# Optimization experiments

Measured on AMD Instinct MI355X. Metric: run time of the kernel, lower is better.

## Reference

```python
import jax, jax.numpy as jnp
import numpy as np
import math

B, S, H = 4, 1024, 1024
E, TOP_K, WINDOW = 4, 2, 64
CONFIGS = [(8, 'standard'), (12, 'standard'), (8, 'linear'), (8, 'local')]
PARAM_NAMES = ['Wq', 'bq', 'Wk', 'bk', 'Wv', 'bv', 'Wo', 'bo']


def setup_inputs() -> dict:
    key = jax.random.key(0)
    ks = jax.random.split(key, 2 + 8 * E)
    d = {}
    d['x'] = jax.random.normal(ks[0], (B, S, H), jnp.float32)
    d['Wg'] = jax.random.normal(ks[1], (H, E), jnp.float32) * 0.02
    i = 2
    for e, (nh, _) in enumerate(CONFIGS):
        hd = H // nh
        pd = nh * hd  # 1020 for nh=12, else 1024
        shapes = [(H, pd), (pd,), (H, pd), (pd,), (H, pd), (pd,), (pd, H), (H,)]
        for nm, shp in zip(PARAM_NAMES, shapes):
            d[f'e{e}_{nm}'] = jax.random.normal(ks[i], shp, jnp.float32) * 0.02
            i += 1
    d['attention_mask'] = jnp.ones((B, S), jnp.int32)
    return d


def _heads(y, nh, hd):
    b, s, _ = y.shape
    return y.reshape(b, s, nh, hd).transpose(0, 2, 1, 3)  # [b, nh, s, hd]


def _attention_expert(x, mask, Wq, bq, Wk, bk, Wv, bv, Wo, bo, nh, atype):
    b, s, _ = x.shape
    hd = Wq.shape[1] // nh
    scale = math.sqrt(hd)
    q = _heads(x @ Wq + bq, nh, hd)
    k = _heads(x @ Wk + bk, nh, hd)
    v = _heads(x @ Wv + bv, nh, hd)
    if atype == 'linear':
        # kernel-trick linear attention; original ignores attention_mask here
        q = jax.nn.elu(q) + 1.0
        k = jax.nn.elu(k) + 1.0
        kv = jnp.einsum('bhsd,bhse->bhde', k, v)
        num = jnp.einsum('bhqd,bhde->bhqe', q, kv)
        den = jnp.einsum('bhqd,bhd->bhq', q, k.sum(axis=2)) + 1e-6
        out = num / den[..., None]
    else:
        scores = jnp.einsum('bhqd,bhkd->bhqk', q, k) / scale
        if atype == 'local':
            idx = jnp.arange(s)
            dist = idx[None, :] - idx[:, None]  # j - i
            local_mask = jnp.abs(dist) <= WINDOW // 2
            scores = jnp.where(local_mask[None, None], scores, -jnp.inf)
        scores = jnp.where(mask[:, None, None, :] == 0, -jnp.inf, scores)
        probs = jax.nn.softmax(scores, axis=-1)
        probs = jnp.where(jnp.isnan(probs), 0.0, probs)  # nan_to_num(nan=0)
        out = jnp.einsum('bhqk,bhkd->bhqd', probs, v)
    out = out.transpose(0, 2, 1, 3).reshape(b, s, -1)
    return out @ Wo + bo


def _forward(x, Wg, eparams, attention_mask):
    b, s, h = x.shape
    # TopKGating (eval mode: no noise). logits -> top_k -> softmax over selected
    logits = x.reshape(-1, h) @ Wg  # [b*s, E]
    top_vals, top_idx = jax.lax.top_k(logits, TOP_K)
    gate_w = jax.nn.softmax(top_vals, axis=-1).reshape(b, s, TOP_K)
    sel = top_idx.reshape(b, s, TOP_K)
    outs = jnp.stack([
        _attention_expert(x, attention_mask, *eparams[e], CONFIGS[e][0], CONFIGS[e][1])
        for e in range(E)
    ], axis=0)  # [E, b, s, h]
    perm = outs.transpose(1, 2, 0, 3)  # [b, s, E, h]
    selected = jnp.take_along_axis(perm, sel[..., None], axis=2)  # [b, s, K, h]
    return (selected * gate_w[..., None]).sum(axis=2)


def reference(x, Wg,
              e0_Wq, e0_bq, e0_Wk, e0_bk, e0_Wv, e0_bv, e0_Wo, e0_bo,
              e1_Wq, e1_bq, e1_Wk, e1_bk, e1_Wv, e1_bv, e1_Wo, e1_bo,
              e2_Wq, e2_bq, e2_Wk, e2_bk, e2_Wv, e2_bv, e2_Wo, e2_bo,
              e3_Wq, e3_bq, e3_Wk, e3_bk, e3_Wv, e3_bv, e3_Wo, e3_bo,
              attention_mask):
    eparams = [
        (e0_Wq, e0_bq, e0_Wk, e0_bk, e0_Wv, e0_bv, e0_Wo, e0_bo),
        (e1_Wq, e1_bq, e1_Wk, e1_bk, e1_Wv, e1_bv, e1_Wo, e1_bo),
        (e2_Wq, e2_bq, e2_Wk, e2_bk, e2_Wv, e2_bv, e2_Wo, e2_bo),
        (e3_Wq, e3_bq, e3_Wk, e3_bk, e3_Wv, e3_bv, e3_Wo, e3_bo),
    ]
    return _forward(x, Wg, eparams, attention_mask)
```

## Files before the change

kernel.cpp:

```cpp
#include <hip/hip_runtime.h>
#include <cmath>

#define B_ 4
#define S_ 1024
#define H_ 1024

typedef short bf16x8 __attribute__((ext_vector_type(8)));
typedef float f32x4 __attribute__((ext_vector_type(4)));
typedef _Float16 half4 __attribute__((ext_vector_type(4)));

__device__ __forceinline__ unsigned short f2bf(float f) {
  unsigned u = __float_as_uint(f);
  u += 0x7fff + ((u >> 16) & 1);
  return (unsigned short)(u >> 16);
}
__device__ __forceinline__ float bf2f(unsigned short h) {
  return __uint_as_float(((unsigned)h) << 16);
}
__device__ __forceinline__ void gld16(const void* g, void* l) {
  __builtin_amdgcn_global_load_lds(
      (const __attribute__((address_space(1))) unsigned int*)g,
      (__attribute__((address_space(3))) unsigned int*)l, 16, 0, 0);
}

__global__ __launch_bounds__(64) void gate_kernel(
    const float* __restrict__ x, const float* __restrict__ Wg,
    float* __restrict__ gw) {
  int t = blockIdx.x;
  int lane = threadIdx.x;
  const float* xr = x + (size_t)t * H_;
  float a0 = 0.f, a1 = 0.f, a2 = 0.f, a3 = 0.f;
  for (int h = lane; h < H_; h += 64) {
    float xv = xr[h];
    const float* wr = Wg + h * 4;
    a0 += xv * wr[0]; a1 += xv * wr[1]; a2 += xv * wr[2]; a3 += xv * wr[3];
  }
  for (int off = 32; off > 0; off >>= 1) {
    a0 += __shfl_down(a0, off);
    a1 += __shfl_down(a1, off);
    a2 += __shfl_down(a2, off);
    a3 += __shfl_down(a3, off);
  }
  if (lane == 0) {
    float v[4] = {a0, a1, a2, a3};
    int i0 = 0; float b0 = v[0];
    for (int e = 1; e < 4; ++e) if (v[e] > b0) { b0 = v[e]; i0 = e; }
    int i1 = -1; float b1 = -INFINITY;
    for (int e = 0; e < 4; ++e) { if (e == i0) continue; if (v[e] > b1) { b1 = v[e]; i1 = e; } }
    float e1v = expf(b1 - b0);
    float w0 = 1.f / (1.f + e1v);
    float w1 = e1v / (1.f + e1v);
    float o[4] = {0.f, 0.f, 0.f, 0.f};
    o[i0] = w0; o[i1] = w1;
    float* g = gw + t * 4;
    g[0] = o[0]; g[1] = o[1]; g[2] = o[2]; g[3] = o[3];
  }
}

__global__ __launch_bounds__(256) void conv_kernel(
    const float* __restrict__ src, unsigned short* __restrict__ dst,
    int nsrc, int ldsrc) {
  int idx = blockIdx.x * 256 + threadIdx.x;
  int m = idx >> 10, c = idx & 1023;
  dst[idx] = (c < nsrc) ? f2bf(src[(size_t)m * ldsrc + c]) : (unsigned short)0;
}

__global__ __launch_bounds__(256) void wtrans4_kernel(
    const float* __restrict__ s0, const float* __restrict__ s1,
    const float* __restrict__ s2, const float* __restrict__ s3,
    unsigned short* __restrict__ d0, unsigned short* __restrict__ d1,
    unsigned short* __restrict__ d2, unsigned short* __restrict__ d3, int pd) {
  __shared__ float tile[32][33];
  int z = blockIdx.z;
  const float* src = (z == 0) ? s0 : (z == 1) ? s1 : (z == 2) ? s2 : s3;
  unsigned short* dst = (z == 0) ? d0 : (z == 1) ? d1 : (z == 2) ? d2 : d3;
  int ksrc = (z < 3) ? 1024 : pd;
  int nsrc = (z < 3) ? pd : 1024;
  int ldsrc = (z < 3) ? pd : 1024;
  int k0 = blockIdx.x * 32, n0 = blockIdx.y * 32;
  int tx = threadIdx.x & 31, ty = threadIdx.x >> 5;
  for (int i = 0; i < 32; i += 8) {
    int k = k0 + ty + i, n = n0 + tx;
    tile[ty + i][tx] = (k < ksrc && n < nsrc) ? src[(size_t)k * ldsrc + n] : 0.f;
  }
  __syncthreads();
  for (int i = 0; i < 32; i += 8) {
    int n = n0 + ty + i, k = k0 + tx;
    dst[(size_t)n * 1024 + k] = f2bf(tile[tx][ty + i]);
  }
}

__global__ __launch_bounds__(256) void gemm_mfma(
    const unsigned short* __restrict__ A, const unsigned short* __restrict__ Bt,
    const float* __restrict__ b0, const float* __restrict__ b1,
    const float* __restrict__ b2, void* __restrict__ Cv, int ldc,
    int nact, int elu_ncut, int out_bf16, int mode,
    const float* __restrict__ gw, int expert, int remap,
    int qs_ncut, float qscale) {
  constexpr int K = 1024;
  __shared__ __align__(16) unsigned short As[128 * 32];
  __shared__ __align__(16) unsigned short Bs[128 * 32];
  int tid = threadIdx.x, wave = tid >> 6, lane = tid & 63;
  int quad = lane >> 4, lrow = lane & 15;
  int rw = (wave >> 1) * 64, cw = (wave & 1) * 64;
  int m0 = blockIdx.y * 128, n0 = blockIdx.x * 128;
  int srow = wave * 32 + (lane >> 2);
  int scol = (lane & 3) * 8;
  const unsigned short* gA = A + (size_t)(m0 + srow) * K + scol;
  const unsigned short* gB = Bt + (size_t)(n0 + srow) * K + scol;
  unsigned short* lA = &As[wave * 1024];
  unsigned short* lB = &Bs[wave * 1024];
  f32x4 acc[4][4];
#pragma unroll
  for (int mt = 0; mt < 4; ++mt)
#pragma unroll
    for (int nt = 0; nt < 4; ++nt) acc[mt][nt] = (f32x4){0.f, 0.f, 0.f, 0.f};

  for (int k0 = 0; k0 < K; k0 += 32) {
    gld16(gA + k0, lA);
    gld16(gA + 16 * K + k0, lA + 512);
    gld16(gB + k0, lB);
    gld16(gB + 16 * K + k0, lB + 512);
    __syncthreads();
    bf16x8 af[4], bfr[4];
#pragma unroll
    for (int t = 0; t < 4; ++t) {
      af[t]  = *(const bf16x8*)&As[(rw + t * 16 + lrow) * 32 + quad * 8];
      bfr[t] = *(const bf16x8*)&Bs[(cw + t * 16 + lrow) * 32 + quad * 8];
    }
#pragma unroll
    for (int mt = 0; mt < 4; ++mt)
#pragma unroll
      for (int nt = 0; nt < 4; ++nt)
        acc[mt][nt] = __builtin_amdgcn_mfma_f32_16x16x32_bf16(
            af[mt], bfr[nt], acc[mt][nt], 0, 0, 0);
    __syncthreads();
  }
#pragma unroll
  for (int nt = 0; nt < 4; ++nt) {
    int n = n0 + cw + nt * 16 + lrow;
    int slice = n >> 10, noff = n & 1023;
    if (noff >= nact) continue;
    const float* bp = (slice == 0) ? b0 : (slice == 1) ? b1 : b2;
    float bias = bp[noff];
    bool do_elu = n < elu_ncut;
    bool do_qs = n < qs_ncut;
    int col = n;
    if (remap) {
      int head = (noff * 12337) >> 20;
      col = slice * 1152 + head * 96 + (noff - head * 85);
    }
#pragma unroll
    for (int mt = 0; mt < 4; ++mt) {
      int mb = m0 + rw + mt * 16 + quad * 4;
#pragma unroll
      for (int r = 0; r < 4; ++r) {
        int m = mb + r;
        float val = acc[mt][nt][r] + bias;
        if (do_elu) val = (val > 0.f) ? val + 1.f : expf(val);
        if (do_qs) val *= qscale;
        size_t ci = (size_t)m * ldc + col;
        if (out_bf16) {
          ((unsigned short*)Cv)[ci] = f2bf(val);
        } else {
          float* C = (float*)Cv;
          if (mode == 0) C[ci] = val;
          else {
            float g = gw[m * 4 + expert];
            if (mode == 1) C[ci] = g * val;
            else           C[ci] += g * val;
          }
        }
      }
    }
  }
}

struct OutP {
  const unsigned short* A[4];
  const unsigned short* B[4];
  const float* bias[4];
};

__global__ __launch_bounds__(256) void gemm_out4(
    OutP p, const float* __restrict__ gw, float* __restrict__ part) {
  constexpr int K = 1024;
  __shared__ __align__(16) unsigned short As[128 * 32];
  __shared__ __align__(16) unsigned short Bs[128 * 32];
  int e = blockIdx.z;
  const unsigned short* A = p.A[e];
  const unsigned short* Bt = p.B[e];
  const float* bp = p.bias[e];
  float* C = part + (size_t)e * (4096ull * 1024ull);
  int tid = threadIdx.x, wave = tid >> 6, lane = tid & 63;
  int quad = lane >> 4, lrow = lane & 15;
  int rw = (wave >> 1) * 64, cw = (wave & 1) * 64;
  int m0 = blockIdx.y * 128, n0 = blockIdx.x * 128;
  int srow = wave * 32 + (lane >> 2);
  int scol = (lane & 3) * 8;
  const unsigned short* gA = A + (size_t)(m0 + srow) * K + scol;
  const unsigned short* gB = Bt + (size_t)(n0 + srow) * K + scol;
  unsigned short* lA = &As[wave * 1024];
  unsigned short* lB = &Bs[wave * 1024];
  f32x4 acc[4][4];
#pragma unroll
  for (int mt = 0; mt < 4; ++mt)
#pragma unroll
    for (int nt = 0; nt < 4; ++nt) acc[mt][nt] = (f32x4){0.f, 0.f, 0.f, 0.f};

  for (int k0 = 0; k0 < K; k0 += 32) {
    gld16(gA + k0, lA);
    gld16(gA + 16 * K + k0, lA + 512);
    gld16(gB + k0, lB);
    gld16(gB + 16 * K + k0, lB + 512);
    __syncthreads();
    bf16x8 af[4], bfr[4];
#pragma unroll
    for (int t = 0; t < 4; ++t) {
      af[t]  = *(const bf16x8*)&As[(rw + t * 16 + lrow) * 32 + quad * 8];
      bfr[t] = *(const bf16x8*)&Bs[(cw + t * 16 + lrow) * 32 + quad * 8];
    }
#pragma unroll
    for (int mt = 0; mt < 4; ++mt)
#pragma unroll
      for (int nt = 0; nt < 4; ++nt)
        acc[mt][nt] = __builtin_amdgcn_mfma_f32_16x16x32_bf16(
            af[mt], bfr[nt], acc[mt][nt], 0, 0, 0);
    __syncthreads();
  }
#pragma unroll
  for (int nt = 0; nt < 4; ++nt) {
    int n = n0 + cw + nt * 16 + lrow;
    float bias = bp[n];
#pragma unroll
    for (int mt = 0; mt < 4; ++mt) {
      int mb = m0 + rw + mt * 16 + quad * 4;
#pragma unroll
      for (int r = 0; r < 4; ++r) {
        int m = mb + r;
        float g = gw[m * 4 + e];
        C[(size_t)m * 1024 + n] = g * (acc[mt][nt][r] + bias);
      }
    }
  }
}

__global__ __launch_bounds__(256) void reduce4(
    const float* __restrict__ part, float* __restrict__ out) {
  constexpr size_t N = 4096ull * 1024ull;
  size_t idx = ((size_t)blockIdx.x * 256 + threadIdx.x) * 4;
  f32x4 a0 = *(const f32x4*)(part + idx);
  f32x4 a1 = *(const f32x4*)(part + idx + N);
  f32x4 a2 = *(const f32x4*)(part + idx + 2 * N);
  f32x4 a3 = *(const f32x4*)(part + idx + 3 * N);
  f32x4 s;
#pragma unroll
  for (int j = 0; j < 4; ++j) {
    float t = a0[j];
    t += a1[j]; t += a2[j]; t += a3[j];
    s[j] = t;
  }
  *(f32x4*)(out + idx) = s;
}

__global__ __launch_bounds__(256) void padzero(
    unsigned short* __restrict__ qkv1, unsigned short* __restrict__ aob1) {
  int idx = blockIdx.x * 256 + threadIdx.x;
  int m = idx / 396, r = idx % 396;
  int slice = r / 132, r2 = r % 132;
  int head = r2 / 11, c = 85 + r2 % 11;
  qkv1[(size_t)m * 3456 + slice * 1152 + head * 96 + c] = 0;
  if (idx < 4096 * 4) {
    int mm = idx >> 2, cc = 1020 + (idx & 3);
    aob1[(size_t)mm * 1024 + cc] = 0;
  }
}

template <int HD, bool LOCAL>
__device__ __forceinline__ void attn_body(
    char* smem,
    const unsigned short* __restrict__ q, const unsigned short* __restrict__ k,
    const unsigned short* __restrict__ v, const int* __restrict__ amask,
    unsigned short* __restrict__ ao, int ldq, int h) {
  constexpr int HDP = (HD + 31) & ~31;
  constexpr int DCH = HDP / 32;
  constexpr int NDT = HDP / 16;
  constexpr int NCH = HDP / 8;
  constexpr int QT = 128, KT = 64;
  constexpr int KLD = HDP + 8;
  constexpr int VLD = KT + 4;
  constexpr int W2 = 32;
  unsigned short* Ks = (unsigned short*)smem;
  _Float16* Vt = (_Float16*)(smem + (size_t)KT * KLD * 2);
  unsigned long long* amq =
      (unsigned long long*)(smem + (size_t)KT * KLD * 2 + (size_t)HDP * VLD * 2);
  int tid = threadIdx.x, wave = tid >> 6, lane = tid & 63;
  int quad = lane >> 4, l15 = lane & 15;
  int q0 = blockIdx.x * QT, b = blockIdx.z;
  size_t baseq = ((size_t)b * S_) * ldq + (size_t)h * HDP;
  size_t baseo = ((size_t)b * S_) * H_ + (size_t)h * HD;

  {
    unsigned long long bb0 = __ballot(amask[b * S_ + wave * 128 + lane] != 0);
    unsigned long long bb1 = __ballot(amask[b * S_ + wave * 128 + 64 + lane] != 0);
    if (lane == 0) { amq[wave * 2] = bb0; amq[wave * 2 + 1] = bb1; }
  }

  int qrow = q0 + wave * 16 + l15;
  bf16x8 qf[DCH];
#pragma unroll
  for (int c = 0; c < DCH; ++c)
#pragma unroll
    for (int j = 0; j < 8; ++j) {
      int d = c * 32 + quad * 8 + j;
      qf[c][j] = (d < HD) ? (short)q[baseq + (size_t)qrow * ldq + d] : (short)0;
    }

  int jlo = 0, jhi = S_;
  if (LOCAL) {
    jlo = q0 - W2; if (jlo < 0) jlo = 0; jlo &= ~(KT - 1);
    jhi = q0 + QT + W2; if (jhi > S_) jhi = S_;
  }

  int skey = tid & 63, sc8a = tid >> 6, sc8b = 8 + (tid >> 6);
  bool sactb = sc8b < NCH;
  const unsigned short* kg = k + baseq + (size_t)skey * ldq;
  const unsigned short* vg = v + baseq + (size_t)skey * ldq;
  bf16x8 kra = {}, krb = {}, vra = {}, vrb = {};
  {
    size_t o = (size_t)jlo * ldq;
    kra = *(const bf16x8*)(kg + o + sc8a * 8);
    vra = *(const bf16x8*)(vg + o + sc8a * 8);
    if (sactb) {
      krb = *(const bf16x8*)(kg + o + sc8b * 8);
      vrb = *(const bf16x8*)(vg + o + sc8b * 8);
    }
  }

  float m_run = -1e30f, l_run = 0.f;
  f32x4 accd[NDT];
#pragma unroll
  for (int dt = 0; dt < NDT; ++dt) accd[dt] = (f32x4){0.f, 0.f, 0.f, 0.f};

  for (int j0 = jlo; j0 < jhi; j0 += KT) {
    __syncthreads();
    *(bf16x8*)&Ks[skey * KLD + sc8a * 8] = kra;
#pragma unroll
    for (int j = 0; j < 8; ++j)
      Vt[(sc8a * 8 + j) * VLD + skey] = (_Float16)bf2f((unsigned short)vra[j]);
    if (sactb) {
      *(bf16x8*)&Ks[skey * KLD + sc8b * 8] = krb;
#pragma unroll
      for (int j = 0; j < 8; ++j)
        Vt[(sc8b * 8 + j) * VLD + skey] = (_Float16)bf2f((unsigned short)vrb[j]);
    }
    __syncthreads();
    int jn = j0 + KT;
    if (jn < jhi) {
      size_t o = (size_t)jn * ldq;
      kra = *(const bf16x8*)(kg + o + sc8a * 8);
      vra = *(const bf16x8*)(vg + o + sc8a * 8);
      if (sactb) {
        krb = *(const bf16x8*)(kg + o + sc8b * 8);
        vrb = *(const bf16x8*)(vg + o + sc8b * 8);
      }
    }
    f32x4 sf[4];
#pragma unroll
    for (int kt = 0; kt < 4; ++kt) {
      sf[kt] = (f32x4){0.f, 0.f, 0.f, 0.f};
#pragma unroll
      for (int c = 0; c < DCH; ++c) {
        bf16x8 kf = *(const bf16x8*)&Ks[(kt * 16 + l15) * KLD + c * 32 + quad * 8];
        sf[kt] = __builtin_amdgcn_mfma_f32_16x16x32_bf16(kf, qf[c], sf[kt], 0, 0, 0);
      }
    }
    unsigned long long mb = amq[j0 >> 6];
    unsigned mw[2] = {(unsigned)mb, (unsigned)(mb >> 32)};
    float sval[4][4];
    bool vld[4][4];
    float mx = -1e30f;
#pragma unroll
    for (int kt = 0; kt < 4; ++kt) {
      unsigned word = mw[kt >> 1];
      int sh = (kt & 1) * 16 + quad * 4;
#pragma unroll
      for (int r = 0; r < 4; ++r) {
        bool ok = (word >> (sh + r)) & 1;
        if (LOCAL) {
          int dj = (j0 + kt * 16 + quad * 4 + r) - qrow;
          ok = ok && (dj <= W2) && (dj >= -W2);
        }
        float s = ok ? sf[kt][r] : -1e30f;
        sval[kt][r] = s;
        vld[kt][r] = ok;
        mx = fmaxf(mx, s);
      }
    }
    mx = fmaxf(mx, __shfl_xor(mx, 16));
    mx = fmaxf(mx, __shfl_xor(mx, 32));
    float m_new = fmaxf(m_run, mx);
    float psum = 0.f;
    float pv[4][4];
#pragma unroll
    for (int kt = 0; kt < 4; ++kt)
#pragma unroll
      for (int r = 0; r < 4; ++r) {
        float p = vld[kt][r] ? __builtin_amdgcn_exp2f(sval[kt][r] - m_new) : 0.f;
        pv[kt][r] = p;
        psum += p;
      }
    psum += __shfl_xor(psum, 16);
    psum += __shfl_xor(psum, 32);
    float alpha = __builtin_amdgcn_exp2f(m_run - m_new);
    m_run = m_new;
    l_run = l_run * alpha + psum;
    float aR[4];
#pragma unroll
    for (int r = 0; r < 4; ++r)
      aR[r] = __shfl(alpha, (lane & 48) | (quad * 4 + r));
#pragma unroll
    for (int dt = 0; dt < NDT; ++dt)
#pragma unroll
      for (int r = 0; r < 4; ++r) accd[dt][r] *= aR[r];
    half4 pf[4];
#pragma unroll
    for (int kt = 0; kt < 4; ++kt)
#pragma unroll
      for (int r = 0; r < 4; ++r) pf[kt][r] = (_Float16)pv[kt][r];
#pragma unroll
    for (int dt = 0; dt < NDT; ++dt)
#pragma unroll
      for (int kt = 0; kt < 4; ++kt) {
        half4 vf = *(const half4*)&Vt[(dt * 16 + l15) * VLD + kt * 16 + quad * 4];
        accd[dt] = __builtin_amdgcn_mfma_f32_16x16x16f16(pf[kt], vf, accd[dt], 0, 0, 0);
      }
  }
  float linv = (l_run > 0.f) ? 1.f / l_run : 0.f;
  float lR[4];
#pragma unroll
  for (int r = 0; r < 4; ++r)
    lR[r] = __shfl(linv, (lane & 48) | (quad * 4 + r));
#pragma unroll
  for (int dt = 0; dt < NDT; ++dt) {
    int d = dt * 16 + l15;
    if (d >= HD) continue;
#pragma unroll
    for (int r = 0; r < 4; ++r) {
      int row = q0 + wave * 16 + quad * 4 + r;
      ao[baseo + (size_t)row * H_ + d] = f2bf(accd[dt][r] * lR[r]);
    }
  }
}

template <int HD, bool LOCAL>
__global__ __launch_bounds__(512) void attn_mfma3(
    const unsigned short* __restrict__ q, const unsigned short* __restrict__ k,
    const unsigned short* __restrict__ v, const int* __restrict__ amask,
    unsigned short* __restrict__ ao, int ldq) {
  constexpr int HDP = (HD + 31) & ~31;
  __shared__ __align__(16) char smem[64 * (HDP + 8) * 2 + HDP * 68 * 2 + 128];
  attn_body<HD, LOCAL>(smem, q, k, v, amask, ao, ldq, blockIdx.y);
}

__global__ __launch_bounds__(512) void attn_mega(
    const unsigned short* __restrict__ qkv0,
    const unsigned short* __restrict__ qkv1,
    const unsigned short* __restrict__ qkv3, const int* __restrict__ amask,
    unsigned short* __restrict__ ao0, unsigned short* __restrict__ ao1,
    unsigned short* __restrict__ ao3) {
  __shared__ __align__(16) char smem[34944];
  int y = blockIdx.y;
  if (y < 8)
    attn_body<128, false>(smem, qkv0, qkv0 + 1024, qkv0 + 2048, amask, ao0,
                          3072, y);
  else if (y < 20)
    attn_body<85, false>(smem, qkv1, qkv1 + 1152, qkv1 + 2304, amask, ao1,
                         3456, y - 8);
  else
    attn_body<128, true>(smem, qkv3, qkv3 + 1024, qkv3 + 2048, amask, ao3,
                         3072, y - 20);
}

#define NSPLIT 4
__global__ __launch_bounds__(256) void linkv_mfma(
    const unsigned short* __restrict__ k, const unsigned short* __restrict__ v,
    float* __restrict__ kvp, float* __restrict__ ksump, int ld) {
  constexpr int HD = 128;
  constexpr int TLD = 34;
  __shared__ __align__(16) unsigned short Kt[HD * TLD];
  __shared__ __align__(16) unsigned short Vt[HD * TLD];
  int h = blockIdx.x, b = blockIdx.y, split = blockIdx.z;
  int bh = b * 8 + h;
  int tid = threadIdx.x, wave = tid >> 6, lane = tid & 63;
  int quad = lane >> 4, l15 = lane & 15;
  int rw = (wave >> 1) * 64, cw = (wave & 1) * 64;
  size_t base = ((size_t)b * S_) * ld + (size_t)h * HD;
  int s_begin = split * (S_ / NSPLIT);

  f32x4 acc[4][4];
#pragma unroll
  for (int mt = 0; mt < 4; ++mt)
#pragma unroll
    for (int nt = 0; nt < 4; ++nt) acc[mt][nt] = (f32x4){0.f, 0.f, 0.f, 0.f};
  float ksacc = 0.f;
  int myd = tid & 127, half = tid >> 7;

  for (int c0 = 0; c0 < S_ / NSPLIT; c0 += 32) {
    for (int idx = tid; idx < 32 * HD; idx += 256) {
      int d = idx & 127, s = idx >> 7;
      size_t g = base + (size_t)(s_begin + c0 + s) * ld + d;
      Kt[d * TLD + s] = k[g];
      Vt[d * TLD + s] = v[g];
    }
    __syncthreads();
    bf16x8 af[4], bf[4];
#pragma unroll
    for (int t = 0; t < 4; ++t) {
      af[t] = *(const bf16x8*)&Vt[(rw + t * 16 + l15) * TLD + quad * 8];
      bf[t] = *(const bf16x8*)&Kt[(cw + t * 16 + l15) * TLD + quad * 8];
    }
#pragma unroll
    for (int mt = 0; mt < 4; ++mt)
#pragma unroll
      for (int nt = 0; nt < 4; ++nt)
        acc[mt][nt] = __builtin_amdgcn_mfma_f32_16x16x32_bf16(
            af[mt], bf[nt], acc[mt][nt], 0, 0, 0);
#pragma unroll
    for (int s = 0; s < 16; ++s)
      ksacc += bf2f(Kt[myd * TLD + half * 16 + s]);
    __syncthreads();
  }
  float* red = (float*)Kt;
  if (half == 1) red[myd] = ksacc;
  __syncthreads();
  if (half == 0)
    ksump[((size_t)split * 32 + bh) * HD + myd] = ksacc + red[myd];
  float* kvo = kvp + ((size_t)split * 32 + bh) * (HD * HD);
#pragma unroll
  for (int mt = 0; mt < 4; ++mt)
#pragma unroll
    for (int nt = 0; nt < 4; ++nt) {
      int dk = cw + nt * 16 + l15;
#pragma unroll
      for (int r = 0; r < 4; ++r) {
        int dv = rw + mt * 16 + quad * 4 + r;
        kvo[(size_t)dv * HD + dk] = acc[mt][nt][r];
      }
    }
}

__global__ __launch_bounds__(256) void linkv_reduce(
    const float* __restrict__ kvp, const float* __restrict__ ksump,
    unsigned short* __restrict__ kvb, float* __restrict__ ksum) {
  int idx = blockIdx.x * 256 + threadIdx.x;
  float s = 0.f;
#pragma unroll
  for (int p = 0; p < NSPLIT; ++p) s += kvp[(size_t)p * (32 * 128 * 128) + idx];
  kvb[idx] = f2bf(s);
  if (idx < 32 * 128) {
    float t = 0.f;
#pragma unroll
    for (int p = 0; p < NSPLIT; ++p) t += ksump[(size_t)p * (32 * 128) + idx];
    ksum[idx] = t;
  }
}

__global__ __launch_bounds__(256) void linattn_mfma(
    const unsigned short* __restrict__ q, const unsigned short* __restrict__ kvT,
    const float* __restrict__ ksum, unsigned short* __restrict__ ao, int ldq) {
  constexpr int KLD = 136;
  __shared__ __align__(16) unsigned short Ks[128 * KLD];
  __shared__ float ksL[128];
  int tid = threadIdx.x, wave = tid >> 6, lane = tid & 63;
  int quad = lane >> 4, l15 = lane & 15;
  int rw = (wave >> 1) * 64, cw = (wave & 1) * 64;
  int q0 = blockIdx.x * 128, h = blockIdx.y, b = blockIdx.z;
  int bh = b * 8 + h;
  size_t baseq = ((size_t)b * S_) * ldq + (size_t)h * 128;
  size_t baseo = ((size_t)b * S_) * H_ + (size_t)h * 128;
  const unsigned short* kvg = kvT + (size_t)bh * (128 * 128);
  for (int idx = tid; idx < 128 * 16; idx += 256) {
    int e = idx >> 4, c = idx & 15;
    *(bf16x8*)&Ks[e * KLD + c * 8] = *(const bf16x8*)&kvg[e * 128 + c * 8];
  }
  if (tid < 128) ksL[tid] = ksum[(size_t)bh * 128 + tid];
  bf16x8 qf[4][4];
#pragma unroll
  for (int mt = 0; mt < 4; ++mt) {
    const unsigned short* qr = q + baseq + (size_t)(q0 + rw + mt * 16 + l15) * ldq;
#pragma unroll
    for (int kc = 0; kc < 4; ++kc)
      qf[mt][kc] = *(const bf16x8*)&qr[kc * 32 + quad * 8];
  }
  __syncthreads();
  f32x4 acc[4][4];
#pragma unroll
  for (int mt = 0; mt < 4; ++mt)
#pragma unroll
    for (int nt = 0; nt < 4; ++nt) acc[mt][nt] = (f32x4){0.f, 0.f, 0.f, 0.f};
#pragma unroll
  for (int kc = 0; kc < 4; ++kc) {
    bf16x8 bf[4];
#pragma unroll
    for (int nt = 0; nt < 4; ++nt)
      bf[nt] = *(const bf16x8*)&Ks[(cw + nt * 16 + l15) * KLD + kc * 32 + quad * 8];
#pragma unroll
    for (int mt = 0; mt < 4; ++mt)
#pragma unroll
      for (int nt = 0; nt < 4; ++nt)
        acc[mt][nt] = __builtin_amdgcn_mfma_f32_16x16x32_bf16(
            qf[mt][kc], bf[nt], acc[mt][nt], 0, 0, 0);
  }
  float den[4];
#pragma unroll
  for (int mt = 0; mt < 4; ++mt) {
    float s = 0.f;
#pragma unroll
    for (int kc = 0; kc < 4; ++kc)
#pragma unroll
      for (int j = 0; j < 8; ++j)
        s += bf2f((unsigned short)qf[mt][kc][j]) * ksL[kc * 32 + quad * 8 + j];
    s += __shfl_xor(s, 16);
    s += __shfl_xor(s, 32);
    den[mt] = s;
  }
#pragma unroll
  for (int mt = 0; mt < 4; ++mt)
#pragma unroll
    for (int r = 0; r < 4; ++r) {
      float dv = __shfl(den[mt], (lane & 48) | (quad * 4 + r));
      float inv = 1.f / (dv + 1e-6f);
      int row = q0 + rw + mt * 16 + quad * 4 + r;
#pragma unroll
      for (int nt = 0; nt < 4; ++nt) {
        int col = cw + nt * 16 + l15;
        ao[baseo + (size_t)row * H_ + col] = f2bf(acc[mt][nt][r] * inv);
      }
    }
}

extern "C" void kernel_launch(void* const* d_in, const int* in_sizes, int n_in,
                              void* d_out, int out_size, void* d_ws, size_t ws_size,
                              hipStream_t stream) {
  const float* x = (const float*)d_in[0];
  const float* Wg = (const float*)d_in[1];
  const int* amask = (const int*)d_in[34];
  float* out = (float*)d_out;
  char* ws = (char*)d_ws;
  const size_t MiB = 1ull << 20;
  const int nhs[4] = {8, 12, 8, 8};
  const float LOG2E = 1.4426950408889634f;

  if (ws_size >= 157 * MiB) {
    float* gw = (float*)ws;
    float* ksum = (float*)(ws + (64ull << 10));
    unsigned short* kvb = (unsigned short*)(ws + 1 * MiB);
    unsigned short* xb = (unsigned short*)(ws + 4 * MiB);
    float* kvp = (float*)(ws + 4 * MiB);
    unsigned short* qkvT = (unsigned short*)(ws + 12 * MiB);
    float* ksump = (float*)(ws + 12 * MiB);
    unsigned short* woT[4];
    for (int e = 0; e < 4; ++e)
      woT[e] = (unsigned short*)(ws + (18 + 2 * e) * MiB);
    const size_t qkvOff[4] = {26 * MiB, 50 * MiB, 77 * MiB, 101 * MiB};
    unsigned short* qkvE[4];
    for (int e = 0; e < 4; ++e) qkvE[e] = (unsigned short*)(ws + qkvOff[e]);
    float* part = (float*)(ws + 26 * MiB);
    unsigned short* aobE[4];
    for (int e = 0; e < 4; ++e)
      aobE[e] = (unsigned short*)(ws + (125 + 8 * e) * MiB);

    conv_kernel<<<16384, 256, 0, stream>>>(x, xb, 1024, 1024);
    gate_kernel<<<4096, 64, 0, stream>>>(x, Wg, gw);
    padzero<<<6336, 256, 0, stream>>>(qkvE[1], aobE[1]);

    for (int e = 0; e < 4; ++e) {
      const float* Wq = (const float*)d_in[2 + 8 * e + 0];
      const float* bq = (const float*)d_in[2 + 8 * e + 1];
      const float* Wk = (const float*)d_in[2 + 8 * e + 2];
      const float* bk = (const float*)d_in[2 + 8 * e + 3];
      const float* Wv = (const float*)d_in[2 + 8 * e + 4];
      const float* bv = (const float*)d_in[2 + 8 * e + 5];
      const float* Wo = (const float*)d_in[2 + 8 * e + 6];
      int nh = nhs[e];
      int hd = H_ / nh;
      int pd = nh * hd;
      int ldqkv = (e == 1) ? 3456 : 3072;
      int qs_ncut = (e == 2) ? 0 : 1024;
      float qscale = LOG2E / sqrtf((float)hd);

      wtrans4_kernel<<<dim3(32, 32, 4), 256, 0, stream>>>(
          Wq, Wk, Wv, Wo, qkvT, qkvT + (1 << 20), qkvT + (2 << 20), woT[e], pd);

      gemm_mfma<<<dim3(24, 32), 256, 0, stream>>>(
          xb, qkvT, bq, bk, bv, qkvE[e], ldqkv,
          (pd == 1020) ? 1020 : 1024, (e == 2) ? 2048 : 0, 1, 0, nullptr, 0,
          (e == 1) ? 1 : 0, qs_ncut, qscale);
    }

    linkv_mfma<<<dim3(8, B_, NSPLIT), 256, 0, stream>>>(
        qkvE[2] + 1024, qkvE[2] + 2048, kvp, ksump, 3072);
    linkv_reduce<<<(32 * 128 * 128) / 256, 256, 0, stream>>>(kvp, ksump, kvb, ksum);
    linattn_mfma<<<dim3(S_ / 128, 8, B_), 256, 0, stream>>>(
        qkvE[2], kvb, ksum, aobE[2], 3072);

    attn_mega<<<dim3(S_ / 128, 28, B_), 512, 0, stream>>>(
        qkvE[0], qkvE[1], qkvE[3], amask, aobE[0], aobE[1], aobE[3]);

    OutP p;
    for (int e = 0; e < 4; ++e) {
      p.A[e] = aobE[e];
      p.B[e] = woT[e];
      p.bias[e] = (const float*)d_in[2 + 8 * e + 7];
    }
    gemm_out4<<<dim3(8, 32, 4), 256, 0, stream>>>(p, gw, part);
    reduce4<<<4096, 256, 0, stream>>>(part, out);
    return;
  }

  float* gw            = (float*)(ws + 0);
  unsigned short* kvb  = (unsigned short*)(ws + (1ull << 20));
  float* ksum          = (float*)(ws + (3ull << 20) + (1ull << 19));
  unsigned short* xb   = (unsigned short*)(ws + (4ull << 20));
  unsigned short* qkvT = (unsigned short*)(ws + (12ull << 20));
  unsigned short* woT  = (unsigned short*)(ws + (18ull << 20));
  unsigned short* qkv  = (unsigned short*)(ws + (20ull << 20));
  unsigned short* aob  = (unsigned short*)(ws + (49ull << 20));
  float* kvp           = (float*)(ws + (57ull << 20));
  float* ksump         = (float*)(ws + (73ull << 20));

  conv_kernel<<<16384, 256, 0, stream>>>(x, xb, 1024, 1024);
  gate_kernel<<<4096, 64, 0, stream>>>(x, Wg, gw);

  for (int e = 0; e < 4; ++e) {
    const float* Wq = (const float*)d_in[2 + 8 * e + 0];
    const float* bq = (const float*)d_in[2 + 8 * e + 1];
    const float* Wk = (const float*)d_in[2 + 8 * e + 2];
    const float* bk = (const float*)d_in[2 + 8 * e + 3];
    const float* Wv = (const float*)d_in[2 + 8 * e + 4];
    const float* bv = (const float*)d_in[2 + 8 * e + 5];
    const float* Wo = (const float*)d_in[2 + 8 * e + 6];
    const float* bo = (const float*)d_in[2 + 8 * e + 7];
    int nh = nhs[e];
    int hd = H_ / nh;
    int pd = nh * hd;
    int ldqkv = (e == 1) ? 3456 : 3072;
    int qs_ncut = (e == 2) ? 0 : 1024;
    float qscale = LOG2E / sqrtf((float)hd);

    wtrans4_kernel<<<dim3(32, 32, 4), 256, 0, stream>>>(
        Wq, Wk, Wv, Wo, qkvT, qkvT + (1 << 20), qkvT + (2 << 20), woT, pd);

    gemm_mfma<<<dim3(24, 32), 256, 0, stream>>>(
        xb, qkvT, bq, bk, bv, qkv, ldqkv,
        (pd == 1020) ? 1020 : 1024, (e == 2) ? 2048 : 0, 1, 0, nullptr, 0,
        (e == 1) ? 1 : 0, qs_ncut, qscale);

    if (e == 2) {
      const unsigned short* qb = qkv;
      const unsigned short* kb = qkv + 1024;
      const unsigned short* vb = qkv + 2048;
      linkv_mfma<<<dim3(8, B_, NSPLIT), 256, 0, stream>>>(kb, vb, kvp, ksump, 3072);
      linkv_reduce<<<(32 * 128 * 128) / 256, 256, 0, stream>>>(kvp, ksump, kvb, ksum);
      linattn_mfma<<<dim3(S_ / 128, 8, B_), 256, 0, stream>>>(qb, kvb, ksum, aob, 3072);
    } else if (e == 1) {
      attn_mfma3<85, false><<<dim3(S_ / 128, 12, B_), 512, 0, stream>>>(
          qkv, qkv + 1152, qkv + 2304, amask, aob, 3456);
    } else if (e == 3) {
      attn_mfma3<128, true><<<dim3(S_ / 128, 8, B_), 512, 0, stream>>>(
          qkv, qkv + 1024, qkv + 2048, amask, aob, 3072);
    } else {
      attn_mfma3<128, false><<<dim3(S_ / 128, 8, B_), 512, 0, stream>>>(
          qkv, qkv + 1024, qkv + 2048, amask, aob, 3072);
    }

    gemm_mfma<<<dim3(8, 32), 256, 0, stream>>>(
        aob, woT, bo, bo, bo, out, 1024, 1024, 0, 0, (e == 0) ? 1 : 2, gw, e, 0,
        0, 1.0f);
  }
}
```

Before: 610.5 us.

## Process two 16-row query groups per wave to double K/V tile reuse

Each wave now handles 32 query rows as two 16-row groups, so a block covers 256 queries and the grid shrinks by half. Each K and V fragment read from shared memory feeds two MFMAs, which halves K/V global loads and LDS staging per query. The cost is more registers for the duplicated Q fragments, accumulators and softmax state, fewer blocks for parallelism (grid 4x28x4 for the mega kernel), and for the local-window case a wider key range per block.

```diff
diff --git a/kernel.cpp b/kernel.cpp
--- a/kernel.cpp
+++ b/kernel.cpp
@@ -286,7 +286,7 @@
   constexpr int DCH = HDP / 32;
   constexpr int NDT = HDP / 16;
   constexpr int NCH = HDP / 8;
-  constexpr int QT = 128, KT = 64;
+  constexpr int QT = 256, KT = 64;
   constexpr int KLD = HDP + 8;
   constexpr int VLD = KT + 4;
   constexpr int W2 = 32;
@@ -306,15 +306,20 @@
     if (lane == 0) { amq[wave * 2] = bb0; amq[wave * 2 + 1] = bb1; }
   }
 
-  int qrow = q0 + wave * 16 + l15;
-  bf16x8 qf[DCH];
-#pragma unroll
-  for (int c = 0; c < DCH; ++c)
-#pragma unroll
-    for (int j = 0; j < 8; ++j) {
-      int d = c * 32 + quad * 8 + j;
-      qf[c][j] = (d < HD) ? (short)q[baseq + (size_t)qrow * ldq + d] : (short)0;
-    }
+  int qrow[2];
+  bf16x8 qf[2][DCH];
+#pragma unroll
+  for (int g = 0; g < 2; ++g) {
+    qrow[g] = q0 + wave * 32 + g * 16 + l15;
+#pragma unroll
+    for (int c = 0; c < DCH; ++c)
+#pragma unroll
+      for (int j = 0; j < 8; ++j) {
+        int d = c * 32 + quad * 8 + j;
+        qf[g][c][j] =
+            (d < HD) ? (short)q[baseq + (size_t)qrow[g] * ldq + d] : (short)0;
+      }
+  }
 
   int jlo = 0, jhi = S_;
   if (LOCAL) {
@@ -337,10 +342,12 @@
     }
   }
 
-  float m_run = -1e30f, l_run = 0.f;
-  f32x4 accd[NDT];
-#pragma unroll
-  for (int dt = 0; dt < NDT; ++dt) accd[dt] = (f32x4){0.f, 0.f, 0.f, 0.f};
+  float m_run[2] = {-1e30f, -1e30f}, l_run[2] = {0.f, 0.f};
+  f32x4 accd[2][NDT];
+#pragma unroll
+  for (int g = 0; g < 2; ++g)
+#pragma unroll
+    for (int dt = 0; dt < NDT; ++dt) accd[g][dt] = (f32x4){0.f, 0.f, 0.f, 0.f};
 
   for (int j0 = jlo; j0 < jhi; j0 += KT) {
     __syncthreads();
@@ -365,90 +372,101 @@
         vrb = *(const bf16x8*)(vg + o + sc8b * 8);
       }
     }
-    f32x4 sf[4];
+    f32x4 sf[2][4];
 #pragma unroll
     for (int kt = 0; kt < 4; ++kt) {
-      sf[kt] = (f32x4){0.f, 0.f, 0.f, 0.f};
+      sf[0][kt] = (f32x4){0.f, 0.f, 0.f, 0.f};
+      sf[1][kt] = (f32x4){0.f, 0.f, 0.f, 0.f};
 #pragma unroll
       for (int c = 0; c < DCH; ++c) {
         bf16x8 kf = *(const bf16x8*)&Ks[(kt * 16 + l15) * KLD + c * 32 + quad * 8];
-        sf[kt] = __builtin_amdgcn_mfma_f32_16x16x32_bf16(kf, qf[c], sf[kt], 0, 0, 0);
+        sf[0][kt] = __builtin_amdgcn_mfma_f32_16x16x32_bf16(kf, qf[0][c], sf[0][kt], 0, 0, 0);
+        sf[1][kt] = __builtin_amdgcn_mfma_f32_16x16x32_bf16(kf, qf[1][c], sf[1][kt], 0, 0, 0);
       }
     }
     unsigned long long mb = amq[j0 >> 6];
     unsigned mw[2] = {(unsigned)mb, (unsigned)(mb >> 32)};
-    float sval[4][4];
-    bool vld[4][4];
-    float mx = -1e30f;
+    float pvv[2][4][4];
+    float mx[2] = {-1e30f, -1e30f};
 #pragma unroll
     for (int kt = 0; kt < 4; ++kt) {
       unsigned word = mw[kt >> 1];
       int sh = (kt & 1) * 16 + quad * 4;
 #pragma unroll
       for (int r = 0; r < 4; ++r) {
-        bool ok = (word >> (sh + r)) & 1;
-        if (LOCAL) {
-          int dj = (j0 + kt * 16 + quad * 4 + r) - qrow;
-          ok = ok && (dj <= W2) && (dj >= -W2);
+        bool okm = (word >> (sh + r)) & 1;
+#pragma unroll
+        for (int g = 0; g < 2; ++g) {
+          bool ok = okm;
+          if (LOCAL) {
+            int dj = (j0 + kt * 16 + quad * 4 + r) - qrow[g];
+            ok = ok && (dj <= W2) && (dj >= -W2);
+          }
+          float s = ok ? sf[g][kt][r] : -1e30f;
+          pvv[g][kt][r] = s;
+          mx[g] = fmaxf(mx[g], s);
         }
-        float s = ok ? sf[kt][r] : -1e30f;
-        sval[kt][r] = s;
-        vld[kt][r] = ok;
-        mx = fmaxf(mx, s);
-      }
-    }
-    mx = fmaxf(mx, __shfl_xor(mx, 16));
-    mx = fmaxf(mx, __shfl_xor(mx, 32));
-    float m_new = fmaxf(m_run, mx);
-    float psum = 0.f;
-    float pv[4][4];
-#pragma unroll
-    for (int kt = 0; kt < 4; ++kt)
-#pragma unroll
-      for (int r = 0; r < 4; ++r) {
-        float p = vld[kt][r] ? __builtin_amdgcn_exp2f(sval[kt][r] - m_new) : 0.f;
-        pv[kt][r] = p;
-        psum += p;
-      }
-    psum += __shfl_xor(psum, 16);
-    psum += __shfl_xor(psum, 32);
-    float alpha = __builtin_amdgcn_exp2f(m_run - m_new);
-    m_run = m_new;
-    l_run = l_run * alpha + psum;
-    float aR[4];
-#pragma unroll
-    for (int r = 0; r < 4; ++r)
-      aR[r] = __shfl(alpha, (lane & 48) | (quad * 4 + r));
-#pragma unroll
-    for (int dt = 0; dt < NDT; ++dt)
-#pragma unroll
-      for (int r = 0; r < 4; ++r) accd[dt][r] *= aR[r];
-    half4 pf[4];
-#pragma unroll
-    for (int kt = 0; kt < 4; ++kt)
-#pragma unroll
-      for (int r = 0; r < 4; ++r) pf[kt][r] = (_Float16)pv[kt][r];
+      }
+    }
+    half4 pf[2][4];
+    float aR[2][4];
+#pragma unroll
+    for (int g = 0; g < 2; ++g) {
+      float mxg = fmaxf(mx[g], __shfl_xor(mx[g], 16));
+      mxg = fmaxf(mxg, __shfl_xor(mxg, 32));
+      float m_new = fmaxf(m_run[g], mxg);
+      float psum = 0.f;
+#pragma unroll
+      for (int kt = 0; kt < 4; ++kt)
+#pragma unroll
+        for (int r = 0; r < 4; ++r) {
+          float s = pvv[g][kt][r];
+          float p = (s > -1e29f) ? __builtin_amdgcn_exp2f(s - m_new) : 0.f;
+          pvv[g][kt][r] = p;
+          psum += p;
+        }
+      psum += __shfl_xor(psum, 16);
+      psum += __shfl_xor(psum, 32);
+      float alpha = __builtin_amdgcn_exp2f(m_run[g] - m_new);
+      m_run[g] = m_new;
+      l_run[g] = l_run[g] * alpha + psum;
+#pragma unroll
+      for (int r = 0; r < 4; ++r)
+        aR[g][r] = __shfl(alpha, (lane & 48) | (quad * 4 + r));
+#pragma unroll
+      for (int dt = 0; dt < NDT; ++dt)
+#pragma unroll
+        for (int r = 0; r < 4; ++r) accd[g][dt][r] *= aR[g][r];
+#pragma unroll
+      for (int kt = 0; kt < 4; ++kt)
+#pragma unroll
+        for (int r = 0; r < 4; ++r) pf[g][kt][r] = (_Float16)pvv[g][kt][r];
+    }
 #pragma unroll
     for (int dt = 0; dt < NDT; ++dt)
 #pragma unroll
       for (int kt = 0; kt < 4; ++kt) {
         half4 vf = *(const half4*)&Vt[(dt * 16 + l15) * VLD + kt * 16 + quad * 4];
-        accd[dt] = __builtin_amdgcn_mfma_f32_16x16x16f16(pf[kt], vf, accd[dt], 0, 0, 0);
-      }
-  }
-  float linv = (l_run > 0.f) ? 1.f / l_run : 0.f;
-  float lR[4];
-#pragma unroll
-  for (int r = 0; r < 4; ++r)
-    lR[r] = __shfl(linv, (lane & 48) | (quad * 4 + r));
-#pragma unroll
-  for (int dt = 0; dt < NDT; ++dt) {
-    int d = dt * 16 + l15;
-    if (d >= HD) continue;
-#pragma unroll
-    for (int r = 0; r < 4; ++r) {
-      int row = q0 + wave * 16 + quad * 4 + r;
-      ao[baseo + (size_t)row * H_ + d] = f2bf(accd[dt][r] * lR[r]);
+        accd[0][dt] = __builtin_amdgcn_mfma_f32_16x16x16f16(pf[0][kt], vf, accd[0][dt], 0, 0, 0);
+        accd[1][dt] = __builtin_amdgcn_mfma_f32_16x16x16f16(pf[1][kt], vf, accd[1][dt], 0, 0, 0);
+      }
+  }
+#pragma unroll
+  for (int g = 0; g < 2; ++g) {
+    float linv = (l_run[g] > 0.f) ? 1.f / l_run[g] : 0.f;
+    float lR[4];
+#pragma unroll
+    for (int r = 0; r < 4; ++r)
+      lR[r] = __shfl(linv, (lane & 48) | (quad * 4 + r));
+#pragma unroll
+    for (int dt = 0; dt < NDT; ++dt) {
+      int d = dt * 16 + l15;
+      if (d >= HD) continue;
+#pragma unroll
+      for (int r = 0; r < 4; ++r) {
+        int row = q0 + wave * 32 + g * 16 + quad * 4 + r;
+        ao[baseo + (size_t)row * H_ + d] = f2bf(accd[g][dt][r] * lR[r]);
+      }
     }
   }
 }
@@ -705,7 +723,7 @@
     linattn_mfma<<<dim3(S_ / 128, 8, B_), 256, 0, stream>>>(
         qkvE[2], kvb, ksum, aobE[2], 3072);
 
-    attn_mega<<<dim3(S_ / 128, 28, B_), 512, 0, stream>>>(
+    attn_mega<<<dim3(S_ / 256, 28, B_), 512, 0, stream>>>(
         qkvE[0], qkvE[1], qkvE[3], amask, aobE[0], aobE[1], aobE[3]);
 
     OutP p;
@@ -765,13 +783,13 @@
       linkv_reduce<<<(32 * 128 * 128) / 256, 256, 0, stream>>>(kvp, ksump, kvb, ksum);
       linattn_mfma<<<dim3(S_ / 128, 8, B_), 256, 0, stream>>>(qb, kvb, ksum, aob, 3072);
     } else if (e == 1) {
-      attn_mfma3<85, false><<<dim3(S_ / 128, 12, B_), 512, 0, stream>>>(
+      attn_mfma3<85, false><<<dim3(S_ / 256, 12, B_), 512, 0, stream>>>(
           qkv, qkv + 1152, qkv + 2304, amask, aob, 3456);
     } else if (e == 3) {
-      attn_mfma3<128, true><<<dim3(S_ / 128, 8, B_), 512, 0, stream>>>(
+      attn_mfma3<128, true><<<dim3(S_ / 256, 8, B_), 512, 0, stream>>>(
           qkv, qkv + 1024, qkv + 2048, amask, aob, 3072);
     } else {
-      attn_mfma3<128, false><<<dim3(S_ / 128, 8, B_), 512, 0, stream>>>(
+      attn_mfma3<128, false><<<dim3(S_ / 256, 8, B_), 512, 0, stream>>>(
           qkv, qkv + 1024, qkv + 2048, amask, aob, 3072);
     }
 
```

After: 593.6 us. 1.03x faster.
